# Optimization experiments

Measured on AMD Instinct MI355X. Metric: run time of the kernel, lower is better.

## Reference

```python
import jax, jax.numpy as jnp
import numpy as np

B, S, DIM, N, D = 1, 3072, 2048, 16, 128
EPS = 1e-06


def rms_norm(x, w, eps=EPS):
    # x: [B, S, C]; normalize over last dim (matches npu_rms_norm)
    var = jnp.mean(jnp.square(x), axis=-1, keepdims=True)
    return x * jax.lax.rsqrt(var + eps) * w


def rope_interleave(x, cos, sin):
    # x: [B, S, N, D]; cos/sin: [B, S, 1, D] with pairwise-repeated values.
    # interleave mode: (x0, x1) -> (x0*c - x1*s, x1*c + x0*s) for adjacent pairs.
    xe = x[..., 0::2]
    xo = x[..., 1::2]
    rot = jnp.stack([-xo, xe], axis=-1).reshape(x.shape)
    return (x * cos + rot * sin).astype(jnp.float32)  # rope_apply casts to float


def setup_inputs() -> dict:
    key = jax.random.key(0)
    ks = jax.random.split(key, 16)
    sd = 1.0 / np.sqrt(DIM)
    inp = {
        'x': jax.random.normal(ks[0], (B, S, DIM), jnp.float32),
        'Wq': jax.random.normal(ks[1], (DIM, DIM), jnp.float32) * sd,
        'bq': jax.random.normal(ks[2], (DIM,), jnp.float32) * 0.01,
        'Wk': jax.random.normal(ks[3], (DIM, DIM), jnp.float32) * sd,
        'bk': jax.random.normal(ks[4], (DIM,), jnp.float32) * 0.01,
        'Wv': jax.random.normal(ks[5], (DIM, DIM), jnp.float32) * sd,
        'bv': jax.random.normal(ks[6], (DIM,), jnp.float32) * 0.01,
        'Wo': jax.random.normal(ks[7], (DIM, DIM), jnp.float32) * sd,
        'bo': jax.random.normal(ks[8], (DIM,), jnp.float32) * 0.01,
        'norm_q_w': jnp.ones((DIM,), jnp.float32),
        'norm_k_w': jnp.ones((DIM,), jnp.float32),
    }
    # per-sample 3D rope folded into precomputed interleaved cos/sin tables
    pos = jnp.arange(S, dtype=jnp.float32)
    inv = 1.0 / (10000.0 ** (jnp.arange(D // 2, dtype=jnp.float32) / (D // 2)))
    ang = pos[:, None] * inv[None, :]                    # [S, D/2]
    cos = jnp.repeat(jnp.cos(ang), 2, axis=-1)           # [S, D] pairwise repeated
    sin = jnp.repeat(jnp.sin(ang), 2, axis=-1)
    inp['rope_cos'] = jnp.broadcast_to(cos[None, :, None, :], (B, S, 1, D))
    inp['rope_sin'] = jnp.broadcast_to(sin[None, :, None, :], (B, S, 1, D))
    inp['seq_lens'] = jax.random.randint(ks[9], (B,), S // 2, S + 1).astype(jnp.int32)
    inp['grid_sizes'] = jnp.broadcast_to(jnp.array([[12, 16, 16]], jnp.int32), (B, 3))
    return inp


def reference(x, Wq, bq, Wk, bk, Wv, bv, Wo, bo, norm_q_w, norm_k_w,
              rope_cos, rope_sin, seq_lens, grid_sizes):
    b, s, _ = x.shape
    # fused QKV projection + RMSNorm on q/k
    q = rms_norm(x @ Wq.T + bq, norm_q_w).reshape(b, s, N, D)
    k = rms_norm(x @ Wk.T + bk, norm_k_w).reshape(b, s, N, D)
    v = (x @ Wv.T + bv).reshape(b, s, N, D)
    # per-sample interleaved RoPE (outputs float32, as in rope_apply)
    q = rope_interleave(q, rope_cos, rope_sin)
    k = rope_interleave(k, rope_cos, rope_sin)
    # full attention with key-length masking (window_size = (-1, -1))
    scale = 1.0 / np.sqrt(D)
    scores = jnp.einsum('bqnd,bknd->bnqk', q, k) * scale    # [B, N, S, S]
    kmask = jnp.arange(s)[None, :] < seq_lens[:, None]       # [B, S]
    scores = jnp.where(kmask[:, None, None, :], scores, jnp.float32(-1e30))
    probs = jax.nn.softmax(scores, axis=-1)
    out = jnp.einsum('bnqk,bknd->bqnd', probs, v.astype(jnp.float32))
    out = out.reshape(b, s, N * D)
    return out @ Wo.T + bo
```

## Files before the change

kernel.cpp:

```cpp
#include <hip/hip_runtime.h>

typedef __attribute__((ext_vector_type(8))) short short8;
typedef __attribute__((ext_vector_type(4))) float f32x4;

#define SQ 3072
#define DM 2048
#define NHEAD 16
#define HDIM 128

__device__ __forceinline__ unsigned short f2bf(float f) {
  union { float f; unsigned int u; } un; un.f = f;
  unsigned int r = un.u + 0x7fffu + ((un.u >> 16) & 1u);
  return (unsigned short)(r >> 16);
}

__device__ __forceinline__ void gload_lds16(const void* g, void* l) {
  __builtin_amdgcn_global_load_lds(
      (const __attribute__((address_space(1))) void*)g,
      (__attribute__((address_space(3))) void*)l, 16, 0, 0);
}

__global__ __launch_bounds__(256) void cvt_all(
    const float* __restrict__ x, const float* __restrict__ wq, const float* __restrict__ wk,
    const float* __restrict__ wv, const float* __restrict__ wo,
    unsigned short* __restrict__ xb, unsigned short* __restrict__ wqkvb,
    unsigned short* __restrict__ wob)
{
  int b = blockIdx.x;
  const float* src; unsigned short* dst; int idx;
  if (b < 3072) { src = x; dst = xb; idx = b; }
  else {
    int r = b - 3072; int w = r >> 11; idx = r & 2047;
    src = (w == 0) ? wq : (w == 1) ? wk : (w == 2) ? wv : wo;
    dst = (w < 3) ? wqkvb + (size_t)w * DM * DM : wob;
  }
  int i = (idx * 256 + threadIdx.x) * 8;
  float4 a = *(const float4*)(src + i);
  float4 c = *(const float4*)(src + i + 4);
  short8 r;
  r[0] = (short)f2bf(a.x); r[1] = (short)f2bf(a.y);
  r[2] = (short)f2bf(a.z); r[3] = (short)f2bf(a.w);
  r[4] = (short)f2bf(c.x); r[5] = (short)f2bf(c.y);
  r[6] = (short)f2bf(c.z); r[7] = (short)f2bf(c.w);
  *(short8*)(dst + i) = r;
}

__global__ __launch_bounds__(256) void gemm_nt_bias(
    const unsigned short* __restrict__ A, const unsigned short* __restrict__ B,
    const float* __restrict__ b0, const float* __restrict__ b1, const float* __restrict__ b2,
    float* __restrict__ C, int M, int N, int K)
{
  __shared__ __align__(16) unsigned short lds[3 * 16384];
  const int tid = threadIdx.x;
  const int wave = tid >> 6, lane = tid & 63;
  const int wm = wave >> 1, wn = wave & 1;
  const int m0 = blockIdx.y * 128, n0 = blockIdx.x * 128;
  const int lr = lane & 15, lg = lane >> 4;

  const int srow = tid >> 3;
  const int ks = (tid & 7) ^ (srow & 7);
  const unsigned short* aSrc = A + (size_t)(m0 + srow) * K + ks * 8;
  const unsigned short* bSrc = B + (size_t)(n0 + srow) * K + ks * 8;
  const int dstOff = (tid & 192) * 8;

  auto stage = [&](int t, int b) {
    const unsigned short* as = aSrc + (size_t)t * 64;
    const unsigned short* bs = bSrc + (size_t)t * 64;
    unsigned short* la = &lds[b * 16384 + dstOff];
    #pragma unroll
    for (int c = 0; c < 4; ++c) {
      gload_lds16(as + (size_t)c * 32 * K, la + c * 2048);
      gload_lds16(bs + (size_t)c * 32 * K, la + 8192 + c * 2048);
    }
  };

  f32x4 acc[4][4] = {};
  const int nt = K >> 6;
  stage(0, 0);
  stage(1, 1);
  asm volatile("s_waitcnt vmcnt(8)\n\ts_barrier" ::: "memory");

  const int sx = lr & 7;
  const int arow = wm * 64 + lr;
  const int brow = wn * 64 + lr;
  for (int t = 0; t < nt; ++t) {
    const unsigned short* La = &lds[(t % 3) * 16384];
    const unsigned short* Lb = La + 8192;
    if (t + 2 < nt) stage(t + 2, (t + 2) % 3);
    short8 af[2][4], bfr[2][4];
    #pragma unroll
    for (int kk = 0; kk < 2; ++kk) {
      #pragma unroll
      for (int m = 0; m < 4; ++m)
        af[kk][m] = *(const short8*)&La[(arow + m * 16) * 64 + (((kk * 4 + lg) ^ sx) << 3)];
      #pragma unroll
      for (int n = 0; n < 4; ++n)
        bfr[kk][n] = *(const short8*)&Lb[(brow + n * 16) * 64 + (((kk * 4 + lg) ^ sx) << 3)];
    }
    __builtin_amdgcn_s_setprio(1);
    #pragma unroll
    for (int kk = 0; kk < 2; ++kk) {
      #pragma unroll
      for (int m = 0; m < 4; ++m) {
        #pragma unroll
        for (int n = 0; n < 4; ++n)
          acc[m][n] = __builtin_amdgcn_mfma_f32_16x16x32_bf16(af[kk][m], bfr[kk][n], acc[m][n], 0, 0, 0);
      }
    }
    __builtin_amdgcn_s_setprio(0);
    if (t + 2 < nt) asm volatile("s_waitcnt vmcnt(8)\n\ts_barrier" ::: "memory");
    else            asm volatile("s_waitcnt vmcnt(0)\n\ts_barrier" ::: "memory");
  }

  const float* bp = (n0 < DM) ? b0 : ((n0 < 2 * DM) ? b1 : b2);
  #pragma unroll
  for (int n = 0; n < 4; ++n) {
    int col = n0 + wn * 64 + n * 16 + lr;
    float bv = bp[col & (DM - 1)];
    #pragma unroll
    for (int m = 0; m < 4; ++m) {
      int row = m0 + wm * 64 + m * 16 + lg * 4;
      #pragma unroll
      for (int j = 0; j < 4; ++j)
        C[(size_t)(row + j) * N + col] = acc[m][n][j] + bv;
    }
  }
}

__global__ __launch_bounds__(256) void normrope(
    const float* __restrict__ qkv, const float* __restrict__ nqw, const float* __restrict__ nkw,
    const float* __restrict__ cosb, const float* __restrict__ sinb,
    unsigned short* __restrict__ Qb, unsigned short* __restrict__ Kb)
{
  const int s = blockIdx.x, z = blockIdx.y;
  const float* row = qkv + ((size_t)s * 3 + z) * DM;
  const float* gw = z ? nkw : nqw;
  unsigned short* ob = z ? Kb : Qb;
  const int t = threadIdx.x;
  float v[8];
  {
    float4 a = *(const float4*)(row + t * 8);
    float4 b = *(const float4*)(row + t * 8 + 4);
    v[0] = a.x; v[1] = a.y; v[2] = a.z; v[3] = a.w;
    v[4] = b.x; v[5] = b.y; v[6] = b.z; v[7] = b.w;
  }
  float ss = 0.f;
  #pragma unroll
  for (int i = 0; i < 8; ++i) ss += v[i] * v[i];
  #pragma unroll
  for (int off = 1; off < 64; off <<= 1) ss += __shfl_xor(ss, off);
  __shared__ float red[4];
  const int wave = t >> 6, lane = t & 63;
  if (lane == 0) red[wave] = ss;
  __syncthreads();
  float tot = red[0] + red[1] + red[2] + red[3];
  float rsc = rsqrtf(tot * (1.0f / 2048.0f) + 1e-6f);
  const float qs = z ? 1.0f : 0.12751879522087045f;
  const int col = t * 8, d = col & 127, h = col >> 7;
  const float* cb = cosb + (size_t)s * HDIM + d;
  const float* sb = sinb + (size_t)s * HDIM + d;
  float y[8];
  #pragma unroll
  for (int i = 0; i < 8; ++i) y[i] = v[i] * rsc * gw[col + i];
  short8 r;
  #pragma unroll
  for (int p = 0; p < 4; ++p) {
    float e = y[2 * p], o = y[2 * p + 1];
    float c0 = cb[2 * p], s0 = sb[2 * p];
    float c1 = cb[2 * p + 1], s1 = sb[2 * p + 1];
    r[2 * p]     = (short)f2bf((e * c0 - o * s0) * qs);
    r[2 * p + 1] = (short)f2bf((o * c1 + e * s1) * qs);
  }
  *(short8*)(ob + ((size_t)h * SQ + s) * HDIM + d) = r;
}

__global__ __launch_bounds__(256) void vtrans(const float* __restrict__ V, int ldv,
                                              unsigned short* __restrict__ Vt)
{
  __shared__ float tile[64][65];
  const int db = blockIdx.x * 64, sb = blockIdx.y * 64, h = blockIdx.z;
  const int t = threadIdx.x;
  const int rr = t >> 2, c0 = (t & 3) * 16;
  const float* src = V + (size_t)(sb + rr) * ldv + h * HDIM + db + c0;
  #pragma unroll
  for (int i = 0; i < 4; ++i) {
    float4 a = *(const float4*)(src + i * 4);
    tile[rr][c0 + i * 4 + 0] = a.x; tile[rr][c0 + i * 4 + 1] = a.y;
    tile[rr][c0 + i * 4 + 2] = a.z; tile[rr][c0 + i * 4 + 3] = a.w;
  }
  __syncthreads();
  const int dr = t >> 2, s0 = (t & 3) * 16;
  short8 r0, r1;
  #pragma unroll
  for (int i = 0; i < 8; ++i) r0[i] = (short)f2bf(tile[s0 + i][dr]);
  #pragma unroll
  for (int i = 0; i < 8; ++i) r1[i] = (short)f2bf(tile[s0 + 8 + i][dr]);
  unsigned short* dst = Vt + ((size_t)h * HDIM + db + dr) * SQ + sb + s0;
  *(short8*)(dst) = r0;
  *(short8*)(dst + 8) = r1;
}

__global__ __launch_bounds__(256) void attn(
    const unsigned short* __restrict__ Qb, const unsigned short* __restrict__ Kb,
    const unsigned short* __restrict__ Vt, const int* __restrict__ seq_lens,
    unsigned short* __restrict__ aout)
{
  __shared__ __align__(16) unsigned short Ks[64 * 136];
  __shared__ __align__(16) unsigned short Vs[128 * 72];
  __shared__ __align__(16) unsigned short Ps[4][16 * 72];
  const int tid = threadIdx.x, wave = tid >> 6, lane = tid & 63;
  const int h = blockIdx.y, q0 = blockIdx.x * 64;
  const int lr = lane & 15, lg = lane >> 4;
  const int seq_len = seq_lens[0];

  short8 qf[4];
  {
    const unsigned short* qrow = Qb + ((size_t)h * SQ + q0 + wave * 16 + lr) * HDIM;
    #pragma unroll
    for (int kk = 0; kk < 4; ++kk)
      qf[kk] = *(const short8*)(qrow + kk * 32 + lg * 8);
  }
  f32x4 o[8] = {};
  float lsum[4] = {0.f, 0.f, 0.f, 0.f};

  for (int kt = 0; kt < seq_len; kt += 64) {
    #pragma unroll
    for (int c = 0; c < 4; ++c) {
      int lin = c * 256 + tid;
      int krow = lin >> 4, kc = (lin & 15) * 8;
      short8 tv = *(const short8*)(Kb + ((size_t)h * SQ + kt + krow) * HDIM + kc);
      *(short8*)&Ks[krow * 136 + kc] = tv;
    }
    #pragma unroll
    for (int c = 0; c < 4; ++c) {
      int lin = c * 256 + tid;
      int vrow = lin >> 3, vc = (lin & 7) * 8;
      short8 tv = *(const short8*)(Vt + ((size_t)h * HDIM + vrow) * SQ + kt + vc);
      *(short8*)&Vs[vrow * 72 + vc] = tv;
    }
    __syncthreads();

    f32x4 sf[4] = {};
    #pragma unroll
    for (int kk = 0; kk < 4; ++kk) {
      #pragma unroll
      for (int n = 0; n < 4; ++n) {
        short8 kf = *(const short8*)&Ks[(n * 16 + lr) * 136 + kk * 32 + lg * 8];
        sf[n] = __builtin_amdgcn_mfma_f32_16x16x32_bf16(qf[kk], kf, sf[n], 0, 0, 0);
      }
    }
    if (kt + 64 > seq_len) {
      #pragma unroll
      for (int n = 0; n < 4; ++n) {
        if (kt + n * 16 + lr >= seq_len) {
          #pragma unroll
          for (int j = 0; j < 4; ++j) sf[n][j] = -3.0e38f;
        }
      }
    }
    unsigned short* Pw = &Ps[wave][0];
    #pragma unroll
    for (int n = 0; n < 4; ++n) {
      #pragma unroll
      for (int j = 0; j < 4; ++j) {
        float p = exp2f(sf[n][j]);
        lsum[j] += p;
        Pw[(lg * 4 + j) * 72 + n * 16 + lr] = f2bf(p);
      }
    }
    #pragma unroll
    for (int kk = 0; kk < 2; ++kk) {
      short8 pa = *(const short8*)&Pw[lr * 72 + kk * 32 + lg * 8];
      #pragma unroll
      for (int dn = 0; dn < 8; ++dn) {
        short8 vb = *(const short8*)&Vs[(dn * 16 + lr) * 72 + kk * 32 + lg * 8];
        o[dn] = __builtin_amdgcn_mfma_f32_16x16x32_bf16(pa, vb, o[dn], 0, 0, 0);
      }
    }
    __syncthreads();
  }
  #pragma unroll
  for (int off = 1; off < 16; off <<= 1) {
    #pragma unroll
    for (int j = 0; j < 4; ++j) lsum[j] += __shfl_xor(lsum[j], off);
  }
  float rcp[4];
  #pragma unroll
  for (int j = 0; j < 4; ++j) rcp[j] = 1.0f / lsum[j];
  #pragma unroll
  for (int dn = 0; dn < 8; ++dn) {
    int col = h * HDIM + dn * 16 + lr;
    #pragma unroll
    for (int j = 0; j < 4; ++j) {
      int row = q0 + wave * 16 + lg * 4 + j;
      aout[(size_t)row * DM + col] = f2bf(o[dn][j] * rcp[j]);
    }
  }
}

extern "C" void kernel_launch(void* const* d_in, const int* in_sizes, int n_in,
                              void* d_out, int out_size, void* d_ws, size_t ws_size,
                              hipStream_t stream) {
  const float* x   = (const float*)d_in[0];
  const float* Wq  = (const float*)d_in[1];
  const float* bq  = (const float*)d_in[2];
  const float* Wk  = (const float*)d_in[3];
  const float* bk  = (const float*)d_in[4];
  const float* Wv  = (const float*)d_in[5];
  const float* bv  = (const float*)d_in[6];
  const float* Wo  = (const float*)d_in[7];
  const float* bo  = (const float*)d_in[8];
  const float* nqw = (const float*)d_in[9];
  const float* nkw = (const float*)d_in[10];
  const float* rc  = (const float*)d_in[11];
  const float* rs  = (const float*)d_in[12];
  const int* seql  = (const int*)d_in[13];
  float* out = (float*)d_out;

  unsigned short* xb   = (unsigned short*)d_ws;
  unsigned short* Wqkv = xb   + (size_t)SQ * DM;
  unsigned short* Wob  = Wqkv + (size_t)3 * DM * DM;
  float* qkv           = (float*)(Wob + (size_t)DM * DM);
  unsigned short* Qb   = (unsigned short*)(qkv + (size_t)3 * SQ * DM);
  unsigned short* Kb   = Qb + (size_t)SQ * DM;
  unsigned short* Vt   = Kb + (size_t)SQ * DM;
  unsigned short* aob  = Vt + (size_t)SQ * DM;

  cvt_all<<<3072 + 4 * 2048, 256, 0, stream>>>(x, Wq, Wk, Wv, Wo, xb, Wqkv, Wob);

  dim3 gq(3 * DM / 128, SQ / 128);
  gemm_nt_bias<<<gq, 256, 0, stream>>>(xb, Wqkv, bq, bk, bv, qkv, SQ, 3 * DM, DM);

  normrope<<<dim3(SQ, 2), 256, 0, stream>>>(qkv, nqw, nkw, rc, rs, Qb, Kb);
  vtrans<<<dim3(2, SQ / 64, NHEAD), 256, 0, stream>>>(qkv + 2 * DM, 3 * DM, Vt);

  attn<<<dim3(SQ / 64, NHEAD), 256, 0, stream>>>(Qb, Kb, Vt, seql, aob);

  dim3 go(DM / 128, SQ / 128);
  gemm_nt_bias<<<go, 256, 0, stream>>>(aob, Wob, bo, bo, bo, out, SQ, DM, DM);
}
```

Measured before the change: 429.8 us.

## Enlarge GEMM tiles to 256x256 with 512 threads, 4-stage pipeline, swizzled grid

```diff
diff --git a/kernel.cpp b/kernel.cpp
--- a/kernel.cpp
+++ b/kernel.cpp
@@ -45,71 +45,72 @@
   *(short8*)(dst + i) = r;
 }
 
-__global__ __launch_bounds__(256) void gemm_nt_bias(
+__global__ __launch_bounds__(512, 2) void gemm_nt_bias(
     const unsigned short* __restrict__ A, const unsigned short* __restrict__ B,
     const float* __restrict__ b0, const float* __restrict__ b1, const float* __restrict__ b2,
-    float* __restrict__ C, int M, int N, int K)
-{
-  __shared__ __align__(16) unsigned short lds[3 * 16384];
+    float* __restrict__ C, int M, int N, int K, int nbm)
+{
+  __shared__ __align__(16) unsigned short lds[4 * 16384];
   const int tid = threadIdx.x;
-  const int wave = tid >> 6, lane = tid & 63;
-  const int wm = wave >> 1, wn = wave & 1;
-  const int m0 = blockIdx.y * 128, n0 = blockIdx.x * 128;
-  const int lr = lane & 15, lg = lane >> 4;
-
-  const int srow = tid >> 3;
-  const int ks = (tid & 7) ^ (srow & 7);
-  const unsigned short* aSrc = A + (size_t)(m0 + srow) * K + ks * 8;
-  const unsigned short* bSrc = B + (size_t)(n0 + srow) * K + ks * 8;
-  const int dstOff = (tid & 192) * 8;
+  const int w = tid >> 6, l = tid & 63;
+  const int wm = w >> 2, wn = w & 3;
+  const int lr = l & 15, lg = l >> 4;
+
+  const int nwg = gridDim.x;
+  const int swz = (blockIdx.x & 7) * (nwg >> 3) + (blockIdx.x >> 3);
+  const int m0 = (swz % nbm) * 256, n0 = (swz / nbm) * 256;
+
+  const int scol = ((l & 3) ^ ((l >> 3) & 3)) * 8;
+  const unsigned short* aS = A + (size_t)(m0 + w * 16 + (l >> 2)) * K + scol;
+  const unsigned short* bS = B + (size_t)(n0 + w * 16 + (l >> 2)) * K + scol;
+  const int ldst = w * 512;
 
   auto stage = [&](int t, int b) {
-    const unsigned short* as = aSrc + (size_t)t * 64;
-    const unsigned short* bs = bSrc + (size_t)t * 64;
-    unsigned short* la = &lds[b * 16384 + dstOff];
-    #pragma unroll
-    for (int c = 0; c < 4; ++c) {
-      gload_lds16(as + (size_t)c * 32 * K, la + c * 2048);
-      gload_lds16(bs + (size_t)c * 32 * K, la + 8192 + c * 2048);
-    }
+    unsigned short* base = &lds[b * 16384];
+    const size_t tc = (size_t)t * 32;
+    gload_lds16(aS + tc, base + ldst);
+    gload_lds16(aS + tc + (size_t)128 * K, base + 4096 + ldst);
+    gload_lds16(bS + tc, base + 8192 + ldst);
+    gload_lds16(bS + tc + (size_t)128 * K, base + 12288 + ldst);
   };
 
-  f32x4 acc[4][4] = {};
-  const int nt = K >> 6;
-  stage(0, 0);
-  stage(1, 1);
-  asm volatile("s_waitcnt vmcnt(8)\n\ts_barrier" ::: "memory");
-
-  const int sx = lr & 7;
-  const int arow = wm * 64 + lr;
-  const int brow = wn * 64 + lr;
+  const int sph = (lg ^ ((lr >> 1) & 3)) * 8;
+  const int aoff = (wm * 128 + lr) * 32 + sph;
+  const int boff = 8192 + (wn * 64 + lr) * 32 + sph;
+
+  f32x4 acc[8][4] = {};
+  const int nt = K >> 5;
+
+  stage(0, 0); stage(1, 1); stage(2, 2);
+  asm volatile("s_waitcnt vmcnt(8)" ::: "memory");
+  __builtin_amdgcn_s_barrier();
+
   for (int t = 0; t < nt; ++t) {
-    const unsigned short* La = &lds[(t % 3) * 16384];
-    const unsigned short* Lb = La + 8192;
-    if (t + 2 < nt) stage(t + 2, (t + 2) % 3);
-    short8 af[2][4], bfr[2][4];
-    #pragma unroll
-    for (int kk = 0; kk < 2; ++kk) {
-      #pragma unroll
-      for (int m = 0; m < 4; ++m)
-        af[kk][m] = *(const short8*)&La[(arow + m * 16) * 64 + (((kk * 4 + lg) ^ sx) << 3)];
+    const unsigned short* buf = &lds[(t & 3) * 16384];
+    if (t + 3 < nt) stage(t + 3, (t + 3) & 3);
+    short8 af[8], bfr[4];
+    #pragma unroll
+    for (int m = 0; m < 8; ++m) af[m] = *(const short8*)&buf[aoff + m * 512];
+    #pragma unroll
+    for (int n = 0; n < 4; ++n) bfr[n] = *(const short8*)&buf[boff + n * 512];
+    __builtin_amdgcn_s_setprio(1);
+    #pragma unroll
+    for (int m = 0; m < 8; ++m) {
       #pragma unroll
       for (int n = 0; n < 4; ++n)
-        bfr[kk][n] = *(const short8*)&Lb[(brow + n * 16) * 64 + (((kk * 4 + lg) ^ sx) << 3)];
-    }
-    __builtin_amdgcn_s_setprio(1);
-    #pragma unroll
-    for (int kk = 0; kk < 2; ++kk) {
-      #pragma unroll
-      for (int m = 0; m < 4; ++m) {
-        #pragma unroll
-        for (int n = 0; n < 4; ++n)
-          acc[m][n] = __builtin_amdgcn_mfma_f32_16x16x32_bf16(af[kk][m], bfr[kk][n], acc[m][n], 0, 0, 0);
-      }
+        acc[m][n] = __builtin_amdgcn_mfma_f32_16x16x32_bf16(af[m], bfr[n], acc[m][n], 0, 0, 0);
     }
     __builtin_amdgcn_s_setprio(0);
-    if (t + 2 < nt) asm volatile("s_waitcnt vmcnt(8)\n\ts_barrier" ::: "memory");
-    else            asm volatile("s_waitcnt vmcnt(0)\n\ts_barrier" ::: "memory");
+    if (t < nt - 3) {
+      asm volatile("s_waitcnt vmcnt(8)" ::: "memory");
+      __builtin_amdgcn_s_barrier();
+    } else if (t == nt - 3) {
+      asm volatile("s_waitcnt vmcnt(4)" ::: "memory");
+      __builtin_amdgcn_s_barrier();
+    } else if (t == nt - 2) {
+      asm volatile("s_waitcnt vmcnt(0)" ::: "memory");
+      __builtin_amdgcn_s_barrier();
+    }
   }
 
   const float* bp = (n0 < DM) ? b0 : ((n0 < 2 * DM) ? b1 : b2);
@@ -118,8 +119,8 @@
     int col = n0 + wn * 64 + n * 16 + lr;
     float bv = bp[col & (DM - 1)];
     #pragma unroll
-    for (int m = 0; m < 4; ++m) {
-      int row = m0 + wm * 64 + m * 16 + lg * 4;
+    for (int m = 0; m < 8; ++m) {
+      int row = m0 + wm * 128 + m * 16 + lg * 4;
       #pragma unroll
       for (int j = 0; j < 4; ++j)
         C[(size_t)(row + j) * N + col] = acc[m][n][j] + bv;
@@ -328,14 +329,14 @@
 
   cvt_all<<<3072 + 4 * 2048, 256, 0, stream>>>(x, Wq, Wk, Wv, Wo, xb, Wqkv, Wob);
 
-  dim3 gq(3 * DM / 128, SQ / 128);
-  gemm_nt_bias<<<gq, 256, 0, stream>>>(xb, Wqkv, bq, bk, bv, qkv, SQ, 3 * DM, DM);
+  gemm_nt_bias<<<(SQ / 256) * (3 * DM / 256), 512, 0, stream>>>(
+      xb, Wqkv, bq, bk, bv, qkv, SQ, 3 * DM, DM, SQ / 256);
 
   normrope<<<dim3(SQ, 2), 256, 0, stream>>>(qkv, nqw, nkw, rc, rs, Qb, Kb);
   vtrans<<<dim3(2, SQ / 64, NHEAD), 256, 0, stream>>>(qkv + 2 * DM, 3 * DM, Vt);
 
   attn<<<dim3(SQ / 64, NHEAD), 256, 0, stream>>>(Qb, Kb, Vt, seql, aob);
 
-  dim3 go(DM / 128, SQ / 128);
-  gemm_nt_bias<<<go, 256, 0, stream>>>(aob, Wob, bo, bo, bo, out, SQ, DM, DM);
-}
+  gemm_nt_bias<<<(SQ / 256) * (DM / 256), 512, 0, stream>>>(
+      aob, Wob, bo, bo, bo, out, SQ, DM, DM, SQ / 256);
+}
```

After: 450.4 us. 1.05x slower.
